# Performance work log

Measured on AMD Instinct MI355X. Metric: run time of the kernel, lower is better.

Reference implementation:

```python
import jax, jax.numpy as jnp
import numpy as np

D_MODEL = 1024
N_HEAD = 16
L, B = 2048, 2


def setup_inputs() -> dict:
    key = jax.random.key(0)
    ks = jax.random.split(key, 11)
    inp = {
        "q": jax.random.normal(ks[0], (L, B, D_MODEL), dtype=jnp.float32),
        "k": jax.random.normal(ks[1], (L, B, D_MODEL), dtype=jnp.float32),
        "v": jax.random.normal(ks[2], (L, B, D_MODEL), dtype=jnp.float32),
        "sph": jax.random.uniform(ks[3], (B, N_HEAD, L, L), dtype=jnp.float32),
        "mask": jax.random.randint(ks[4], (B, L, L), 0, 2, dtype=jnp.int32),
        # learned params (torch Linear stores W of shape [out, in]; y = x @ W.T)
        "Wq": jax.random.normal(ks[5], (D_MODEL, D_MODEL), dtype=jnp.float32) * (1.0 / np.sqrt(D_MODEL)),
        "Wk": jax.random.normal(ks[6], (D_MODEL, D_MODEL), dtype=jnp.float32) * (1.0 / np.sqrt(D_MODEL)),
        "Wv": jax.random.normal(ks[7], (D_MODEL, D_MODEL), dtype=jnp.float32) * (1.0 / np.sqrt(D_MODEL)),
        "Wfc": jax.random.normal(ks[8], (D_MODEL, D_MODEL), dtype=jnp.float32) * (1.0 / np.sqrt(D_MODEL)),
        "gamma": jnp.ones((D_MODEL,), dtype=jnp.float32),
        "beta": jnp.zeros((D_MODEL,), dtype=jnp.float32),
    }
    return inp


def reference(q, k, v, sph, mask, Wq, Wk, Wv, Wfc, gamma, beta):
    # q, k, v: [L, B, D]  ->  batch-first [B, L, D]
    n_head = N_HEAD
    Lq, Bb, D = q.shape
    d_k = D // n_head
    x_q = jnp.transpose(q, (1, 0, 2))
    x_k = jnp.transpose(k, (1, 0, 2))
    x_v = jnp.transpose(v, (1, 0, 2))
    residual = x_q  # [B, L, D]

    # projections (no bias), split heads: [B, H, L, d_k]
    qh = (x_q @ Wq.T).reshape(Bb, Lq, n_head, d_k).transpose(0, 2, 1, 3)
    kh = (x_k @ Wk.T).reshape(Bb, Lq, n_head, d_k).transpose(0, 2, 1, 3)
    vh = (x_v @ Wv.T).reshape(Bb, Lq, n_head, d_k).transpose(0, 2, 1, 3)

    scale = jnp.asarray(d_k, qh.dtype) ** 0.5
    attn = jnp.einsum('bhqd,bhkd->bhqk', qh / scale, kh)
    attn = attn * sph                                   # spatial decay modulation
    attn = jnp.where(mask[:, None, :, :] == 0, jnp.asarray(-1e9, attn.dtype), attn)
    p_attn = jax.nn.softmax(attn, axis=-1)              # dropout is identity in eval

    out = jnp.einsum('bhqk,bhkd->bhqd', p_attn, vh)     # [B, H, L, d_k]
    out = out.transpose(0, 2, 1, 3).reshape(Bb, Lq, D)
    out = out @ Wfc.T + residual                        # fc (no bias) + residual

    # LayerNorm(eps=1e-6)
    mu = jnp.mean(out, axis=-1, keepdims=True)
    var = jnp.var(out, axis=-1, keepdims=True)
    out = (out - mu) * jax.lax.rsqrt(var + 1e-6) * gamma + beta

    return jnp.transpose(out, (1, 0, 2)), p_attn
```

## Files before the change

kernel.cpp:

```cpp
#include <hip/hip_runtime.h>
#include <hip/hip_bf16.h>

#define LL 2048
#define BB 2
#define DD 1024
#define HH 16
#define DKk 64

typedef __attribute__((ext_vector_type(8))) short s8v;
typedef __attribute__((ext_vector_type(8))) unsigned short u8v;
typedef __attribute__((ext_vector_type(4))) float f4v;

__device__ __forceinline__ ushort f2b(float f){
  union { __hip_bfloat16 h; ushort u; } c; c.h = __float2bfloat16(f); return c.u;
}
__device__ __forceinline__ float b2f(ushort u){
  union { __hip_bfloat16 h; ushort u; } c; c.u = u; return __bfloat162float(c.h);
}
__device__ __forceinline__ f4v nt4(const float* p){ return __builtin_nontemporal_load((const f4v*)p); }
__device__ __forceinline__ void nts4(float* p, f4v v){ __builtin_nontemporal_store(v, (f4v*)p); }

__global__ __launch_bounds__(256) void pack_x_kernel(
    const float* __restrict__ q, const float* __restrict__ k, const float* __restrict__ v,
    ushort* __restrict__ xq, ushort* __restrict__ xk, ushort* __restrict__ xv){
  int t = blockIdx.x*256 + threadIdx.x;
  int m = t >> 7;
  int dc = (t & 127) << 3;
  int b = m >> 11, l = m & (LL-1);
  size_t src = ((size_t)(l*BB + b) << 10) + dc;
  size_t dst = ((size_t)m << 10) + dc;
  #pragma unroll
  for (int i=0;i<3;++i){
    const float* ss = (i==0)?q:(i==1)?k:v;
    ushort* dd = (i==0)?xq:(i==1)?xk:xv;
    float4 a = *(const float4*)(ss+src);
    float4 bb = *(const float4*)(ss+src+4);
    u8v o;
    o[0]=f2b(a.x); o[1]=f2b(a.y); o[2]=f2b(a.z); o[3]=f2b(a.w);
    o[4]=f2b(bb.x);o[5]=f2b(bb.y);o[6]=f2b(bb.z);o[7]=f2b(bb.w);
    *(u8v*)(dd+dst) = o;
  }
}

__global__ __launch_bounds__(256) void pack_w_kernel(
    const float* __restrict__ Wq, const float* __restrict__ Wk,
    const float* __restrict__ Wv, const float* __restrict__ Wfc,
    ushort* __restrict__ wb){
  int t = blockIdx.x*256 + threadIdx.x;
  int which = t >> 17;
  size_t idx = (size_t)(t & 131071) << 3;
  const float* s = (which==0)?Wq:(which==1)?Wk:(which==2)?Wv:Wfc;
  float4 a = *(const float4*)(s+idx);
  float4 b4 = *(const float4*)(s+idx+4);
  u8v o;
  o[0]=f2b(a.x);o[1]=f2b(a.y);o[2]=f2b(a.z);o[3]=f2b(a.w);
  o[4]=f2b(b4.x);o[5]=f2b(b4.y);o[6]=f2b(b4.z);o[7]=f2b(b4.w);
  *(u8v*)(wb + ((size_t)which<<20) + idx) = o;
}

__global__ __launch_bounds__(256) void pack_mask_kernel(
    const int* __restrict__ mask, unsigned char* __restrict__ mbits){
  int t = blockIdx.x*256 + threadIdx.x;
  const int* src = mask + ((size_t)t<<3);
  int4 a = *(const int4*)src; int4 b = *(const int4*)(src+4);
  unsigned m = (a.x&1) | ((a.y&1)<<1) | ((a.z&1)<<2) | ((a.w&1)<<3)
             | ((b.x&1)<<4) | ((b.y&1)<<5) | ((b.z&1)<<6) | ((b.w&1)<<7);
  mbits[t] = (unsigned char)m;
}

__device__ __forceinline__ void gemm_body(
    const ushort* __restrict__ A, const ushort* __restrict__ W,
    ushort* __restrict__ outb, float* __restrict__ outf, const float* __restrict__ resid,
    int mode, float scale){
  __shared__ ushort As[4096];
  __shared__ ushort Bs[4096];
  int tid = threadIdx.x;
  int w = tid>>6, lane = tid&63, lane15 = lane&15, g = lane>>4;
  int m0 = blockIdx.y<<7, n0 = blockIdx.x<<7;
  int wr = w>>1, wc = w&1;
  f4v z4 = {0.f,0.f,0.f,0.f};
  f4v acc[4][4];
  #pragma unroll
  for (int i=0;i<4;++i)
    #pragma unroll
    for (int j=0;j<4;++j) acc[i][j] = z4;

  int f0 = tid, f1 = 256 + tid;
  int r0 = f0>>2, c0 = (f0&3)<<3;
  int r1 = f1>>2, c1 = (f1&3)<<3;
  for (int k0=0; k0<1024; k0+=32){
    *(s8v*)&As[(r0<<5)+c0] = *(const s8v*)&A[((size_t)(m0+r0)<<10) + k0 + c0];
    *(s8v*)&As[(r1<<5)+c1] = *(const s8v*)&A[((size_t)(m0+r1)<<10) + k0 + c1];
    *(s8v*)&Bs[(r0<<5)+c0] = *(const s8v*)&W[((size_t)(n0+r0)<<10) + k0 + c0];
    *(s8v*)&Bs[(r1<<5)+c1] = *(const s8v*)&W[((size_t)(n0+r1)<<10) + k0 + c1];
    __syncthreads();
    s8v af[4], bf_[4];
    #pragma unroll
    for (int mi=0;mi<4;++mi) af[mi] = *(s8v*)&As[((wr*64 + mi*16 + lane15)<<5) + (g<<3)];
    #pragma unroll
    for (int ni=0;ni<4;++ni) bf_[ni] = *(s8v*)&Bs[((wc*64 + ni*16 + lane15)<<5) + (g<<3)];
    #pragma unroll
    for (int mi=0;mi<4;++mi)
      #pragma unroll
      for (int ni=0;ni<4;++ni)
        acc[mi][ni] = __builtin_amdgcn_mfma_f32_16x16x32_bf16(af[mi], bf_[ni], acc[mi][ni], 0,0,0);
    __syncthreads();
  }
  #pragma unroll
  for (int mi=0;mi<4;++mi){
    #pragma unroll
    for (int ni=0;ni<4;++ni){
      int mbase = m0 + wr*64 + mi*16 + (g<<2);
      int ncol  = n0 + wc*64 + ni*16 + lane15;
      if (mode==0){
        int b=mbase>>11, h=ncol>>6, j=ncol&63;
        size_t o = (((size_t)(b*HH+h)*LL + (mbase&2047))<<6) + j;
        #pragma unroll
        for (int r=0;r<4;++r) outb[o + ((size_t)r<<6)] = f2b(acc[mi][ni][r]*scale);
      } else if (mode==2){
        int b=mbase>>11, h=ncol>>6, j=ncol&63;
        ushort4 pk = make_ushort4(f2b(acc[mi][ni][0]), f2b(acc[mi][ni][1]),
                                  f2b(acc[mi][ni][2]), f2b(acc[mi][ni][3]));
        *(ushort4*)&outb[(((size_t)(b*HH+h)*DKk + j)<<11) + (mbase&2047)] = pk;
      } else {
        int b=mbase>>11, l2=mbase&2047;
        #pragma unroll
        for (int r=0;r<4;++r)
          outf[((size_t)(mbase+r)<<10)+ncol] =
              acc[mi][ni][r] + resid[((size_t)((l2+r)*BB + b)<<10) + ncol];
      }
    }
  }
}

__global__ __launch_bounds__(256) void gemm_qkv_kernel(
    const ushort* __restrict__ xq, const ushort* __restrict__ xk, const ushort* __restrict__ xv,
    const ushort* __restrict__ wb, ushort* __restrict__ Qh, ushort* __restrict__ Kh, ushort* __restrict__ Vt){
  int z = blockIdx.z;
  const ushort* A = (z==0)?xq:(z==1)?xk:xv;
  const ushort* W = wb + ((size_t)z<<20);
  ushort* outb = (z==0)?Qh:(z==1)?Kh:Vt;
  int mode = (z==2)?2:0;
  float scale = (z==0)?0.125f:1.0f;
  gemm_body(A, W, outb, nullptr, nullptr, mode, scale);
}

__global__ __launch_bounds__(256) void gemm_fc_kernel(
    const ushort* __restrict__ ao, const ushort* __restrict__ wfc,
    const float* __restrict__ resid, float* __restrict__ fco){
  gemm_body(ao, wfc, nullptr, fco, resid, 3, 1.0f);
}

__global__ __launch_bounds__(1024, 8) void attn_kernel(
    const ushort* __restrict__ Qh, const ushort* __restrict__ Kh, const ushort* __restrict__ Vt,
    const float* __restrict__ sph, const unsigned char* __restrict__ mbits,
    float* __restrict__ p_out, ushort* __restrict__ attn_out){
  extern __shared__ char smem[];
  float* pbuf   = (float*)(smem + 65536);
  float* redsum = (float*)(smem + 65536 + 13056);
  int tid = threadIdx.x, w = tid>>6, lane = tid&63, lane15 = lane&15, g = lane>>4;
  int bid = blockIdx.x;
  int qt = bid & 127, h = (bid>>7)&15, b = bid>>11;
  int q0 = qt<<4;
  size_t bh = (size_t)b*HH + h;

  const ushort* Qbase = Qh + ((bh*LL + q0 + lane15)<<6) + (g<<3);
  s8v qa0 = *(const s8v*)Qbase;
  s8v qa1 = *(const s8v*)(Qbase + 32);
  const ushort* Kp = Kh + ((bh*LL + (w<<7) + lane15)<<6) + (g<<3);
  s8v kb0n = *(const s8v*)Kp;
  s8v kb1n = *(const s8v*)(Kp + 32);
  #pragma unroll
  for (int cc=0; cc<8; ++cc){
    s8v kb0 = kb0n, kb1 = kb1n;
    if (cc<7){
      kb0n = *(const s8v*)(Kp + ((cc+1)<<10));
      kb1n = *(const s8v*)(Kp + ((cc+1)<<10) + 32);
    }
    f4v cacc = {0.f,0.f,0.f,0.f};
    cacc = __builtin_amdgcn_mfma_f32_16x16x32_bf16(qa0, kb0, cacc, 0,0,0);
    cacc = __builtin_amdgcn_mfma_f32_16x16x32_bf16(qa1, kb1, cacc, 0,0,0);
    int colb = (((w<<3)+cc)<<5) + (lane15<<1);
    #pragma unroll
    for (int r=0;r<4;++r){
      int row = (g<<2)+r;
      *(ushort*)(smem + (row<<12) + (colb ^ ((row&7)<<4))) = f2b(cacc[r]);
    }
  }
  __syncthreads();

  int row = w;
  int qrow = q0 + row;
  const float* sph_r = sph + ((bh*LL + qrow)<<11);
  const unsigned char* mb_r = mbits + (((size_t)b*LL + qrow)<<8);
  int rswz = (row&7)<<4;
  char* Srow = smem + (row<<12);
  int colbase = lane<<3;
  unsigned mw = (unsigned)mb_r[lane] | ((unsigned)mb_r[lane+64]<<8)
              | ((unsigned)mb_r[lane+128]<<16) | ((unsigned)mb_r[lane+192]<<24);
  f4v a0 = nt4(sph_r + colbase), a1 = nt4(sph_r + colbase + 4);
  s8v svn = *(s8v*)(Srow + ((colbase<<1) ^ rswz));
  float sum = 0.f;
  #pragma unroll
  for (int c2=0;c2<4;++c2){
    f4v p0 = a0, p1 = a1; s8v sv = svn;
    if (c2<3){
      int ncol = colbase + ((c2+1)<<9);
      a0 = nt4(sph_r + ncol); a1 = nt4(sph_r + ncol + 4);
      svn = *(s8v*)(Srow + ((ncol<<1) ^ rswz));
    }
    unsigned m8 = (mw >> (c2*8));
    float e[8];
    e[0] = (m8&1)   ? __expf(b2f((ushort)sv[0])*p0[0]) : 0.f;
    e[1] = (m8&2)   ? __expf(b2f((ushort)sv[1])*p0[1]) : 0.f;
    e[2] = (m8&4)   ? __expf(b2f((ushort)sv[2])*p0[2]) : 0.f;
    e[3] = (m8&8)   ? __expf(b2f((ushort)sv[3])*p0[3]) : 0.f;
    e[4] = (m8&16)  ? __expf(b2f((ushort)sv[4])*p1[0]) : 0.f;
    e[5] = (m8&32)  ? __expf(b2f((ushort)sv[5])*p1[1]) : 0.f;
    e[6] = (m8&64)  ? __expf(b2f((ushort)sv[6])*p1[2]) : 0.f;
    e[7] = (m8&128) ? __expf(b2f((ushort)sv[7])*p1[3]) : 0.f;
    u8v ov;
    #pragma unroll
    for (int j=0;j<8;++j){ sum += e[j]; ov[j] = f2b(e[j]); }
    *(u8v*)(Srow + (((colbase + (c2<<9))<<1) ^ rswz)) = ov;
  }
  #pragma unroll
  for (int off=1; off<64; off<<=1) sum += __shfl_xor(sum, off, 64);
  if (lane==0) redsum[row] = sum;

  float inv = 1.0f / sum;
  float* prow_p = p_out + ((bh*LL + qrow)<<11);
  s8v rv[4];
  #pragma unroll
  for (int c2=0;c2<4;++c2)
    rv[c2] = *(s8v*)(Srow + (((colbase + (c2<<9))<<1) ^ rswz));
  #pragma unroll
  for (int c2=0;c2<4;++c2){
    int col = colbase + (c2<<9);
    f4v o0, o1;
    o0[0]=b2f((ushort)rv[c2][0])*inv; o0[1]=b2f((ushort)rv[c2][1])*inv;
    o0[2]=b2f((ushort)rv[c2][2])*inv; o0[3]=b2f((ushort)rv[c2][3])*inv;
    o1[0]=b2f((ushort)rv[c2][4])*inv; o1[1]=b2f((ushort)rv[c2][5])*inv;
    o1[2]=b2f((ushort)rv[c2][6])*inv; o1[3]=b2f((ushort)rv[c2][7])*inv;
    nts4(prow_p + col, o0);
    nts4(prow_p + col + 4, o1);
  }
  __syncthreads();

  int ds = w & 3, kq = w >> 2;
  f4v oacc = {0.f,0.f,0.f,0.f};
  const ushort* Vb = Vt + ((bh*DKk + (ds<<4) + lane15)<<11) + (kq<<9) + (g<<3);
  char* Sa = smem + (lane15<<12);
  int aswz = (lane15&7)<<4;
  s8v pan = *(s8v*)(Sa + (((kq<<10) + (g<<4)) ^ aswz));
  s8v vbn = *(const s8v*)Vb;
  #pragma unroll
  for (int it=0; it<16; ++it){
    s8v pa = pan, vb = vbn;
    if (it<15){
      pan = *(s8v*)(Sa + (((kq<<10) + ((it+1)<<6) + (g<<4)) ^ aswz));
      vbn = *(const s8v*)(Vb + ((it+1)<<5));
    }
    oacc = __builtin_amdgcn_mfma_f32_16x16x32_bf16(pa, vb, oacc, 0,0,0);
  }
  if (kq){
    float* pp = pbuf + ((kq-1)*1088);
    #pragma unroll
    for (int r=0;r<4;++r) pp[((g<<2)+r)*68 + (ds<<4) + lane15] = oacc[r];
  }
  __syncthreads();
  if (kq==0){
    #pragma unroll
    for (int p=0;p<3;++p){
      float* pp = pbuf + p*1088;
      #pragma unroll
      for (int r=0;r<4;++r) oacc[r] += pp[((g<<2)+r)*68 + (ds<<4) + lane15];
    }
    #pragma unroll
    for (int r=0;r<4;++r){
      int qr = (g<<2)+r;
      float val = oacc[r] / redsum[qr];
      attn_out[((size_t)(b*LL + q0 + qr)<<10) + (h<<6) + (ds<<4) + lane15] = f2b(val);
    }
  }
}

__global__ __launch_bounds__(256) void ln_kernel(const float* __restrict__ fc,
    const float* __restrict__ gamma, const float* __restrict__ beta, float* __restrict__ out){
  __shared__ float rs[4], rq[4];
  int m = blockIdx.x, tid = threadIdx.x;
  int d0 = tid<<2;
  float4 x = *(const float4*)(fc + ((size_t)m<<10) + d0);
  float s = x.x+x.y+x.z+x.w;
  float sq = x.x*x.x+x.y*x.y+x.z*x.z+x.w*x.w;
  #pragma unroll
  for (int off=32; off; off>>=1){ s += __shfl_xor(s,off,64); sq += __shfl_xor(sq,off,64); }
  if ((tid&63)==0){ rs[tid>>6]=s; rq[tid>>6]=sq; }
  __syncthreads();
  float ts = rs[0]+rs[1]+rs[2]+rs[3];
  float tq = rq[0]+rq[1]+rq[2]+rq[3];
  float mu = ts*(1.0f/1024.0f);
  float var = tq*(1.0f/1024.0f) - mu*mu;
  float rr = rsqrtf(var + 1e-6f);
  float4 gm = *(const float4*)(gamma + d0);
  float4 bt = *(const float4*)(beta + d0);
  float4 y;
  y.x=(x.x-mu)*rr*gm.x+bt.x;
  y.y=(x.y-mu)*rr*gm.y+bt.y;
  y.z=(x.z-mu)*rr*gm.z+bt.z;
  y.w=(x.w-mu)*rr*gm.w+bt.w;
  int b=m>>11, l2=m&2047;
  *(float4*)(out + ((size_t)(l2*BB+b)<<10) + d0) = y;
}

extern "C" void kernel_launch(void* const* d_in, const int* in_sizes, int n_in,
                              void* d_out, int out_size, void* d_ws, size_t ws_size,
                              hipStream_t stream){
  const float* q    = (const float*)d_in[0];
  const float* k    = (const float*)d_in[1];
  const float* v    = (const float*)d_in[2];
  const float* sph  = (const float*)d_in[3];
  const int*   mask = (const int*)d_in[4];
  const float* Wq   = (const float*)d_in[5];
  const float* Wk   = (const float*)d_in[6];
  const float* Wv   = (const float*)d_in[7];
  const float* Wfc  = (const float*)d_in[8];
  const float* gamma= (const float*)d_in[9];
  const float* beta = (const float*)d_in[10];
  float* outp  = (float*)d_out;
  float* p_out = outp + 4194304;

  char* ws = (char*)d_ws;
  ushort* xq  = (ushort*)(ws);
  ushort* xk  = (ushort*)(ws + 8388608);
  ushort* xv  = (ushort*)(ws + 16777216);
  ushort* wb  = (ushort*)(ws + 25165824);
  ushort* Qh  = (ushort*)(ws + 33554432);
  ushort* Kh  = (ushort*)(ws + 41943040);
  ushort* Vt  = (ushort*)(ws + 50331648);
  ushort* ao  = (ushort*)(ws + 58720256);
  float*  fco = (float*)(ws + 67108864);
  unsigned char* mbits = (unsigned char*)(ws + 83886080);

  pack_x_kernel<<<2048,256,0,stream>>>(q,k,v,xq,xk,xv);
  pack_w_kernel<<<2048,256,0,stream>>>(Wq,Wk,Wv,Wfc,wb);
  pack_mask_kernel<<<4096,256,0,stream>>>(mask, mbits);
  gemm_qkv_kernel<<<dim3(8,32,3),256,0,stream>>>(xq,xk,xv,wb,Qh,Kh,Vt);
  attn_kernel<<<4096,1024,78784,stream>>>(Qh,Kh,Vt,sph,mbits,p_out,ao);
  gemm_fc_kernel<<<dim3(8,32),256,0,stream>>>(ao, wb + 3145728, q, fco);
  ln_kernel<<<4096,256,0,stream>>>(fco, gamma, beta, outp);
}
```

Baseline: 517.4 us.

## Merge pack kernels and prefetch sph, mask and V earlier in attention

The three packing kernels are merged into one launch that branches on block index, removing two kernel launches. In the attention kernel, the whole sph row and the mask bits are loaded up front so they are in flight during the QK^T MFMA phase. The exp values are kept in registers instead of being reread from shared memory, and V operands are prefetched before the barrier with a 4-deep register ring. This raises register pressure in a 1024-thread block, which could force spills or lower occupancy.

```diff
diff --git a/kernel.cpp b/kernel.cpp
--- a/kernel.cpp
+++ b/kernel.cpp
@@ -20,52 +20,51 @@
 __device__ __forceinline__ f4v nt4(const float* p){ return __builtin_nontemporal_load((const f4v*)p); }
 __device__ __forceinline__ void nts4(float* p, f4v v){ __builtin_nontemporal_store(v, (f4v*)p); }
 
-__global__ __launch_bounds__(256) void pack_x_kernel(
+__global__ __launch_bounds__(256) void pack_all_kernel(
     const float* __restrict__ q, const float* __restrict__ k, const float* __restrict__ v,
-    ushort* __restrict__ xq, ushort* __restrict__ xk, ushort* __restrict__ xv){
-  int t = blockIdx.x*256 + threadIdx.x;
-  int m = t >> 7;
-  int dc = (t & 127) << 3;
-  int b = m >> 11, l = m & (LL-1);
-  size_t src = ((size_t)(l*BB + b) << 10) + dc;
-  size_t dst = ((size_t)m << 10) + dc;
-  #pragma unroll
-  for (int i=0;i<3;++i){
-    const float* ss = (i==0)?q:(i==1)?k:v;
-    ushort* dd = (i==0)?xq:(i==1)?xk:xv;
-    float4 a = *(const float4*)(ss+src);
-    float4 bb = *(const float4*)(ss+src+4);
-    u8v o;
-    o[0]=f2b(a.x); o[1]=f2b(a.y); o[2]=f2b(a.z); o[3]=f2b(a.w);
-    o[4]=f2b(bb.x);o[5]=f2b(bb.y);o[6]=f2b(bb.z);o[7]=f2b(bb.w);
-    *(u8v*)(dd+dst) = o;
-  }
-}
-
-__global__ __launch_bounds__(256) void pack_w_kernel(
     const float* __restrict__ Wq, const float* __restrict__ Wk,
     const float* __restrict__ Wv, const float* __restrict__ Wfc,
-    ushort* __restrict__ wb){
-  int t = blockIdx.x*256 + threadIdx.x;
-  int which = t >> 17;
-  size_t idx = (size_t)(t & 131071) << 3;
-  const float* s = (which==0)?Wq:(which==1)?Wk:(which==2)?Wv:Wfc;
-  float4 a = *(const float4*)(s+idx);
-  float4 b4 = *(const float4*)(s+idx+4);
-  u8v o;
-  o[0]=f2b(a.x);o[1]=f2b(a.y);o[2]=f2b(a.z);o[3]=f2b(a.w);
-  o[4]=f2b(b4.x);o[5]=f2b(b4.y);o[6]=f2b(b4.z);o[7]=f2b(b4.w);
-  *(u8v*)(wb + ((size_t)which<<20) + idx) = o;
-}
-
-__global__ __launch_bounds__(256) void pack_mask_kernel(
-    const int* __restrict__ mask, unsigned char* __restrict__ mbits){
-  int t = blockIdx.x*256 + threadIdx.x;
-  const int* src = mask + ((size_t)t<<3);
-  int4 a = *(const int4*)src; int4 b = *(const int4*)(src+4);
-  unsigned m = (a.x&1) | ((a.y&1)<<1) | ((a.z&1)<<2) | ((a.w&1)<<3)
-             | ((b.x&1)<<4) | ((b.y&1)<<5) | ((b.z&1)<<6) | ((b.w&1)<<7);
-  mbits[t] = (unsigned char)m;
+    const int* __restrict__ mask,
+    ushort* __restrict__ xq, ushort* __restrict__ xk, ushort* __restrict__ xv,
+    ushort* __restrict__ wb, unsigned char* __restrict__ mbits){
+  int blk = blockIdx.x;
+  if (blk < 2048){
+    int t = blk*256 + threadIdx.x;
+    int m = t >> 7;
+    int dc = (t & 127) << 3;
+    int b = m >> 11, l = m & (LL-1);
+    size_t src = ((size_t)(l*BB + b) << 10) + dc;
+    size_t dst = ((size_t)m << 10) + dc;
+    #pragma unroll
+    for (int i=0;i<3;++i){
+      const float* ss = (i==0)?q:(i==1)?k:v;
+      ushort* dd = (i==0)?xq:(i==1)?xk:xv;
+      float4 a = *(const float4*)(ss+src);
+      float4 bb = *(const float4*)(ss+src+4);
+      u8v o;
+      o[0]=f2b(a.x); o[1]=f2b(a.y); o[2]=f2b(a.z); o[3]=f2b(a.w);
+      o[4]=f2b(bb.x);o[5]=f2b(bb.y);o[6]=f2b(bb.z);o[7]=f2b(bb.w);
+      *(u8v*)(dd+dst) = o;
+    }
+  } else if (blk < 4096){
+    int t = (blk-2048)*256 + threadIdx.x;
+    int which = t >> 17;
+    size_t idx = (size_t)(t & 131071) << 3;
+    const float* s = (which==0)?Wq:(which==1)?Wk:(which==2)?Wv:Wfc;
+    float4 a = *(const float4*)(s+idx);
+    float4 b4 = *(const float4*)(s+idx+4);
+    u8v o;
+    o[0]=f2b(a.x);o[1]=f2b(a.y);o[2]=f2b(a.z);o[3]=f2b(a.w);
+    o[4]=f2b(b4.x);o[5]=f2b(b4.y);o[6]=f2b(b4.z);o[7]=f2b(b4.w);
+    *(u8v*)(wb + ((size_t)which<<20) + idx) = o;
+  } else {
+    int t = (blk-4096)*256 + threadIdx.x;
+    const int* src = mask + ((size_t)t<<3);
+    int4 a = *(const int4*)src; int4 b = *(const int4*)(src+4);
+    unsigned m = (a.x&1) | ((a.y&1)<<1) | ((a.z&1)<<2) | ((a.w&1)<<3)
+               | ((b.x&1)<<4) | ((b.y&1)<<5) | ((b.z&1)<<6) | ((b.w&1)<<7);
+    mbits[t] = (unsigned char)m;
+  }
 }
 
 __device__ __forceinline__ void gemm_body(
@@ -163,52 +162,51 @@
   int qt = bid & 127, h = (bid>>7)&15, b = bid>>11;
   int q0 = qt<<4;
   size_t bh = (size_t)b*HH + h;
+  int row = w;
+  int qrow = q0 + row;
+
+  const float* sph_r = sph + ((bh*LL + qrow)<<11);
+  int colbase = lane<<3;
+  f4v sp[8];
+  #pragma unroll
+  for (int c2=0;c2<4;++c2){
+    sp[2*c2]   = nt4(sph_r + colbase + (c2<<9));
+    sp[2*c2+1] = nt4(sph_r + colbase + (c2<<9) + 4);
+  }
+  const unsigned char* mb_r = mbits + (((size_t)b*LL + qrow)<<8);
+  unsigned mw = (unsigned)mb_r[lane] | ((unsigned)mb_r[lane+64]<<8)
+              | ((unsigned)mb_r[lane+128]<<16) | ((unsigned)mb_r[lane+192]<<24);
 
   const ushort* Qbase = Qh + ((bh*LL + q0 + lane15)<<6) + (g<<3);
   s8v qa0 = *(const s8v*)Qbase;
   s8v qa1 = *(const s8v*)(Qbase + 32);
   const ushort* Kp = Kh + ((bh*LL + (w<<7) + lane15)<<6) + (g<<3);
-  s8v kb0n = *(const s8v*)Kp;
-  s8v kb1n = *(const s8v*)(Kp + 32);
   #pragma unroll
   for (int cc=0; cc<8; ++cc){
-    s8v kb0 = kb0n, kb1 = kb1n;
-    if (cc<7){
-      kb0n = *(const s8v*)(Kp + ((cc+1)<<10));
-      kb1n = *(const s8v*)(Kp + ((cc+1)<<10) + 32);
-    }
+    const ushort* Kb = Kp + (cc<<10);
+    s8v kb0 = *(const s8v*)Kb;
+    s8v kb1 = *(const s8v*)(Kb + 32);
     f4v cacc = {0.f,0.f,0.f,0.f};
     cacc = __builtin_amdgcn_mfma_f32_16x16x32_bf16(qa0, kb0, cacc, 0,0,0);
     cacc = __builtin_amdgcn_mfma_f32_16x16x32_bf16(qa1, kb1, cacc, 0,0,0);
     int colb = (((w<<3)+cc)<<5) + (lane15<<1);
     #pragma unroll
     for (int r=0;r<4;++r){
-      int row = (g<<2)+r;
-      *(ushort*)(smem + (row<<12) + (colb ^ ((row&7)<<4))) = f2b(cacc[r]);
+      int rr2 = (g<<2)+r;
+      *(ushort*)(smem + (rr2<<12) + (colb ^ ((rr2&7)<<4))) = f2b(cacc[r]);
     }
   }
   __syncthreads();
 
-  int row = w;
-  int qrow = q0 + row;
-  const float* sph_r = sph + ((bh*LL + qrow)<<11);
-  const unsigned char* mb_r = mbits + (((size_t)b*LL + qrow)<<8);
   int rswz = (row&7)<<4;
   char* Srow = smem + (row<<12);
-  int colbase = lane<<3;
-  unsigned mw = (unsigned)mb_r[lane] | ((unsigned)mb_r[lane+64]<<8)
-              | ((unsigned)mb_r[lane+128]<<16) | ((unsigned)mb_r[lane+192]<<24);
-  f4v a0 = nt4(sph_r + colbase), a1 = nt4(sph_r + colbase + 4);
-  s8v svn = *(s8v*)(Srow + ((colbase<<1) ^ rswz));
   float sum = 0.f;
+  u8v ev[4];
   #pragma unroll
   for (int c2=0;c2<4;++c2){
-    f4v p0 = a0, p1 = a1; s8v sv = svn;
-    if (c2<3){
-      int ncol = colbase + ((c2+1)<<9);
-      a0 = nt4(sph_r + ncol); a1 = nt4(sph_r + ncol + 4);
-      svn = *(s8v*)(Srow + ((ncol<<1) ^ rswz));
-    }
+    int boff = (((colbase + (c2<<9))<<1) ^ rswz);
+    s8v sv = *(s8v*)(Srow + boff);
+    f4v p0 = sp[2*c2], p1 = sp[2*c2+1];
     unsigned m8 = (mw >> (c2*8));
     float e[8];
     e[0] = (m8&1)   ? __expf(b2f((ushort)sv[0])*p0[0]) : 0.f;
@@ -222,7 +220,8 @@
     u8v ov;
     #pragma unroll
     for (int j=0;j<8;++j){ sum += e[j]; ov[j] = f2b(e[j]); }
-    *(u8v*)(Srow + (((colbase + (c2<<9))<<1) ^ rswz)) = ov;
+    ev[c2] = ov;
+    *(u8v*)(Srow + boff) = ov;
   }
   #pragma unroll
   for (int off=1; off<64; off<<=1) sum += __shfl_xor(sum, off, 64);
@@ -230,38 +229,36 @@
 
   float inv = 1.0f / sum;
   float* prow_p = p_out + ((bh*LL + qrow)<<11);
-  s8v rv[4];
-  #pragma unroll
-  for (int c2=0;c2<4;++c2)
-    rv[c2] = *(s8v*)(Srow + (((colbase + (c2<<9))<<1) ^ rswz));
   #pragma unroll
   for (int c2=0;c2<4;++c2){
     int col = colbase + (c2<<9);
     f4v o0, o1;
-    o0[0]=b2f((ushort)rv[c2][0])*inv; o0[1]=b2f((ushort)rv[c2][1])*inv;
-    o0[2]=b2f((ushort)rv[c2][2])*inv; o0[3]=b2f((ushort)rv[c2][3])*inv;
-    o1[0]=b2f((ushort)rv[c2][4])*inv; o1[1]=b2f((ushort)rv[c2][5])*inv;
-    o1[2]=b2f((ushort)rv[c2][6])*inv; o1[3]=b2f((ushort)rv[c2][7])*inv;
+    o0[0]=b2f((ushort)ev[c2][0])*inv; o0[1]=b2f((ushort)ev[c2][1])*inv;
+    o0[2]=b2f((ushort)ev[c2][2])*inv; o0[3]=b2f((ushort)ev[c2][3])*inv;
+    o1[0]=b2f((ushort)ev[c2][4])*inv; o1[1]=b2f((ushort)ev[c2][5])*inv;
+    o1[2]=b2f((ushort)ev[c2][6])*inv; o1[3]=b2f((ushort)ev[c2][7])*inv;
     nts4(prow_p + col, o0);
     nts4(prow_p + col + 4, o1);
   }
+
+  int ds = w & 3, kq = w >> 2;
+  const ushort* Vb = Vt + ((bh*DKk + (ds<<4) + lane15)<<11) + (kq<<9) + (g<<3);
+  s8v vb[4];
+  #pragma unroll
+  for (int i=0;i<4;++i) vb[i] = *(const s8v*)(Vb + (i<<5));
   __syncthreads();
 
-  int ds = w & 3, kq = w >> 2;
   f4v oacc = {0.f,0.f,0.f,0.f};
-  const ushort* Vb = Vt + ((bh*DKk + (ds<<4) + lane15)<<11) + (kq<<9) + (g<<3);
   char* Sa = smem + (lane15<<12);
   int aswz = (lane15&7)<<4;
   s8v pan = *(s8v*)(Sa + (((kq<<10) + (g<<4)) ^ aswz));
-  s8v vbn = *(const s8v*)Vb;
   #pragma unroll
   for (int it=0; it<16; ++it){
-    s8v pa = pan, vb = vbn;
-    if (it<15){
-      pan = *(s8v*)(Sa + (((kq<<10) + ((it+1)<<6) + (g<<4)) ^ aswz));
-      vbn = *(const s8v*)(Vb + ((it+1)<<5));
-    }
-    oacc = __builtin_amdgcn_mfma_f32_16x16x32_bf16(pa, vb, oacc, 0,0,0);
+    s8v pa = pan;
+    if (it<15) pan = *(s8v*)(Sa + (((kq<<10) + ((it+1)<<6) + (g<<4)) ^ aswz));
+    s8v vcur = vb[it&3];
+    if (it<12) vb[it&3] = *(const s8v*)(Vb + ((it+4)<<5));
+    oacc = __builtin_amdgcn_mfma_f32_16x16x32_bf16(pa, vcur, oacc, 0,0,0);
   }
   if (kq){
     float* pp = pbuf + ((kq-1)*1088);
@@ -342,9 +339,7 @@
   float*  fco = (float*)(ws + 67108864);
   unsigned char* mbits = (unsigned char*)(ws + 83886080);
 
-  pack_x_kernel<<<2048,256,0,stream>>>(q,k,v,xq,xk,xv);
-  pack_w_kernel<<<2048,256,0,stream>>>(Wq,Wk,Wv,Wfc,wb);
-  pack_mask_kernel<<<4096,256,0,stream>>>(mask, mbits);
+  pack_all_kernel<<<8192,256,0,stream>>>(q,k,v,Wq,Wk,Wv,Wfc,mask,xq,xk,xv,wb,mbits);
   gemm_qkv_kernel<<<dim3(8,32,3),256,0,stream>>>(xq,xk,xv,wb,Qh,Kh,Vt);
   attn_kernel<<<4096,1024,78784,stream>>>(Qh,Kh,Vt,sph,mbits,p_out,ao);
   gemm_fc_kernel<<<dim3(8,32),256,0,stream>>>(ao, wb + 3145728, q, fco);
```

Result: slower. 532.8 us (+3.0%).
